# Performance work log

Hardware: AMD Instinct MI355X
Metric: run time of the kernel (lower is better)

## Reference

```python
import jax, jax.numpy as jnp
import numpy as np

EPS = 1e-6
STEPS = 6  # eval_steps == train_steps == 6


def _l2norm(v, axis, eps=1e-12):
    # F.normalize: v / max(||v||, eps)
    return v / jnp.maximum(jnp.linalg.norm(v, axis=axis, keepdims=True), eps)


def _conv1x1(x, w, b=None):
    # x: [B,C,H,W], w: [O,C]
    y = jnp.einsum('bchw,oc->bohw', x, w)
    if b is not None:
        y = y + b[None, :, None, None]
    return y


def _nmf_local_inference(x, bases):
    # x: [B,D,N], bases: [B,D,R]; torch.no_grad loop
    coef = jax.nn.softmax(jnp.einsum('bdn,bdr->bnr', x, bases), axis=-1)  # inv_t = 1

    def step(carry, _):
        bases, coef = carry
        # coef update
        xtb = jnp.einsum('bdn,bdr->bnr', x, bases)
        btb = jnp.einsum('bdr,bds->brs', bases, bases)
        coef = coef * xtb / (jnp.einsum('bnr,brs->bns', coef, btb) + EPS)
        # bases update
        xc = jnp.einsum('bdn,bnr->bdr', x, coef)
        ctc = jnp.einsum('bnr,bns->brs', coef, coef)
        bases = bases * xc / (jnp.einsum('bdr,brs->bds', bases, ctc) + EPS)
        return (bases, coef), None

    (bases, coef), _ = jax.lax.scan(step, (bases, coef), None, length=STEPS)
    return bases, coef


def _nmf_compute_coef(x, bases, coef):
    # differentiable final coef refinement
    xtb = jnp.einsum('bdn,bdr->bnr', x, bases)
    btb = jnp.einsum('bdr,bds->brs', bases, bases)
    return coef * xtb / (jnp.einsum('bnr,brs->bns', coef, btb) + EPS)


def _ham_nmf(h, bases0):
    # h: [B,C,H,W], S=1 -> D=C, N=H*W
    B, C, H, W = h.shape
    x = h.reshape(B, C, H * W)
    sg = jax.lax.stop_gradient
    bases, coef = _nmf_local_inference(sg(x), bases0)
    bases, coef = sg(bases), sg(coef)
    coef = _nmf_compute_coef(x, bases, coef)
    out = jnp.einsum('bdr,bnr->bdn', bases, coef)  # bases @ coef^T
    return out.reshape(B, C, H, W)


def reference(x, bases0, w_lower, b_lower, w_cheese, b_cheese, w_upper,
              coef_shortcut, coef_ham):
    shortcut = x
    # lower bread: 1x1 conv + ReLU (NMF variant)
    h = jax.nn.relu(_conv1x1(x, w_lower, b_lower))
    # hamburger (NMF2D, spatial=True, rand_init bases normalized over D)
    bases = _l2norm(bases0, axis=1)
    h = _ham_nmf(h, bases)
    # cheese: 1x1 conv + ReLU (norm_cfg=None -> conv has bias)
    h = jax.nn.relu(_conv1x1(h, w_cheese, b_cheese))
    # upper bread: 1x1 conv, no bias
    h = _conv1x1(h, w_upper)
    return jax.nn.relu(coef_ham * h + coef_shortcut * shortcut)


def setup_inputs() -> dict:
    key = jax.random.key(0)
    ks = jax.random.split(key, 8)
    B, in_c, Hh, Ww = 8, 512, 64, 64
    C, R = 512, 64
    std = (2.0 / C) ** 0.5  # kaiming-style init from _init_weight (1x1 convs)
    std_up = (2.0 / in_c) ** 0.5
    return {
        'x': jax.random.normal(ks[0], (B, in_c, Hh, Ww), jnp.float32),
        'bases0': jax.random.uniform(ks[1], (B, C, R), jnp.float32),
        'w_lower': jax.random.normal(ks[2], (C, in_c), jnp.float32) * std,
        'b_lower': jnp.zeros((C,), jnp.float32),
        'w_cheese': jax.random.normal(ks[3], (C, C), jnp.float32) * std,
        'b_cheese': jnp.zeros((C,), jnp.float32),
        'w_upper': jax.random.normal(ks[4], (in_c, C), jnp.float32) * std_up,
        'coef_shortcut': jnp.ones((1,), jnp.float32),
        'coef_ham': jnp.ones((1,), jnp.float32),
    }
```

## Files before the change

### kernel.cpp

```cpp
#include <hip/hip_runtime.h>

#define NMF_EPS 1e-6f

typedef unsigned short ushort_t;
typedef __attribute__((ext_vector_type(8))) short bf16x8;
typedef __attribute__((ext_vector_type(4))) float f32x4;

__device__ __forceinline__ ushort_t f2bf(float f) {
    unsigned int u = __float_as_uint(f);
    return (ushort_t)((u + 0x7FFFu + ((u >> 16) & 1u)) >> 16);
}
__device__ __forceinline__ float bf2f(ushort_t h) {
    return __uint_as_float(((unsigned int)h) << 16);
}

__device__ __forceinline__ void gl_lds16(const ushort_t* g, ushort_t* l) {
    __builtin_amdgcn_global_load_lds(
        (const __attribute__((address_space(1))) unsigned int*)g,
        (__attribute__((address_space(3))) unsigned int*)l,
        16, 0, 0);
}

template<int SPLIT, int EPI>
__global__ __launch_bounds__(256) void mfma_gemm(
    const ushort_t* __restrict__ Ah, const ushort_t* __restrict__ Al,
    const ushort_t* __restrict__ Bh, const ushort_t* __restrict__ Bl,
    float* __restrict__ C, ushort_t* __restrict__ Chi, ushort_t* __restrict__ Clo,
    int M, int N, int K,
    long sB, long sC,
    const float* __restrict__ bias,
    const float* __restrict__ res, long sRes,
    const float* __restrict__ hamp, const float* __restrict__ scp)
{
    constexpr int SB = SPLIT ? 32768 : 16384;
    __shared__ char smem[2 * SB];

    const int tid  = threadIdx.x;
    const int wave = tid >> 6, lane = tid & 63;
    const int quad = lane >> 4, lr = lane & 15;
    const int batch = blockIdx.z;
    const int m0 = blockIdx.y * 128, n0 = blockIdx.x * 128;

    const ushort_t* Bhb = Bh + (long)batch * sB;
    const ushort_t* Blb = SPLIT ? (Bl + (long)batch * sB) : nullptr;

    f32x4 acc[4][4];
    #pragma unroll
    for (int i = 0; i < 4; ++i)
        #pragma unroll
        for (int j = 0; j < 4; ++j)
            acc[i][j] = (f32x4){0.f, 0.f, 0.f, 0.f};

    const int q   = wave * 2;
    const int ra0 = (q + 0) * 16 + (lane >> 2);
    const int ra1 = (q + 1) * 16 + (lane >> 2);
    const int ko  = (lane & 3) * 8;
    const int wm = (wave & 1) * 64, wn = (wave >> 1) * 64;

    auto STAGE = [&](int buf, int k0) {
        char* base = smem + buf * SB;
        ushort_t* dAh = (ushort_t*)base;
        ushort_t* dBh = (ushort_t*)(base + 8192);
        gl_lds16(&Ah [(long)(m0 + ra0) * K + k0 + ko], &dAh[(q + 0) * 512]);
        gl_lds16(&Ah [(long)(m0 + ra1) * K + k0 + ko], &dAh[(q + 1) * 512]);
        gl_lds16(&Bhb[(long)(n0 + ra0) * K + k0 + ko], &dBh[(q + 0) * 512]);
        gl_lds16(&Bhb[(long)(n0 + ra1) * K + k0 + ko], &dBh[(q + 1) * 512]);
        if constexpr (SPLIT) {
            ushort_t* dAl = (ushort_t*)(base + 16384);
            ushort_t* dBl = (ushort_t*)(base + 24576);
            gl_lds16(&Al [(long)(m0 + ra0) * K + k0 + ko], &dAl[(q + 0) * 512]);
            gl_lds16(&Al [(long)(m0 + ra1) * K + k0 + ko], &dAl[(q + 1) * 512]);
            gl_lds16(&Blb[(long)(n0 + ra0) * K + k0 + ko], &dBl[(q + 0) * 512]);
            gl_lds16(&Blb[(long)(n0 + ra1) * K + k0 + ko], &dBl[(q + 1) * 512]);
        }
    };

    STAGE(0, 0);
    __syncthreads();
    int cur = 0;

    for (int k0 = 0; k0 < K; k0 += 32) {
        if (k0 + 32 < K) STAGE(cur ^ 1, k0 + 32);

        char* base = smem + cur * SB;
        ushort_t* sAh = (ushort_t*)base;
        ushort_t* sBh = (ushort_t*)(base + 8192);

        bf16x8 af[4], bfr[4], afl[4], bfl[4];
        #pragma unroll
        for (int i = 0; i < 4; ++i)
            af[i] = *(const bf16x8*)&sAh[(wm + i * 16 + lr) * 32 + quad * 8];
        #pragma unroll
        for (int j = 0; j < 4; ++j)
            bfr[j] = *(const bf16x8*)&sBh[(wn + j * 16 + lr) * 32 + quad * 8];
        if constexpr (SPLIT) {
            ushort_t* sAl = (ushort_t*)(base + 16384);
            ushort_t* sBl = (ushort_t*)(base + 24576);
            #pragma unroll
            for (int i = 0; i < 4; ++i)
                afl[i] = *(const bf16x8*)&sAl[(wm + i * 16 + lr) * 32 + quad * 8];
            #pragma unroll
            for (int j = 0; j < 4; ++j)
                bfl[j] = *(const bf16x8*)&sBl[(wn + j * 16 + lr) * 32 + quad * 8];
        }

        #pragma unroll
        for (int i = 0; i < 4; ++i)
            #pragma unroll
            for (int j = 0; j < 4; ++j) {
                acc[i][j] = __builtin_amdgcn_mfma_f32_16x16x32_bf16(af[i], bfr[j], acc[i][j], 0, 0, 0);
                if constexpr (SPLIT) {
                    acc[i][j] = __builtin_amdgcn_mfma_f32_16x16x32_bf16(af[i], bfl[j], acc[i][j], 0, 0, 0);
                    acc[i][j] = __builtin_amdgcn_mfma_f32_16x16x32_bf16(afl[i], bfr[j], acc[i][j], 0, 0, 0);
                }
            }
        __syncthreads();
        cur ^= 1;
    }

    if (EPI == 2) {
        ushort_t* Hh = Chi + (long)batch * sC;
        ushort_t* Hl = Clo + (long)batch * sC;
        unsigned int* slab = (unsigned int*)smem;
        #pragma unroll
        for (int p = 0; p < 2; ++p) {
            __syncthreads();
            if ((wave & 1) == p) {
                #pragma unroll
                for (int i = 0; i < 4; ++i) {
                    const int mb = m0 + p * 64 + i * 16 + quad * 4;
                    #pragma unroll
                    for (int j = 0; j < 4; ++j) {
                        const int nl = wn + j * 16 + lr;
                        #pragma unroll
                        for (int r = 0; r < 4; ++r) {
                            float v = fmaxf(acc[i][j][r] + bias[mb + r], 0.f);
                            ushort_t h = f2bf(v);
                            ushort_t l = f2bf(v - bf2f(h));
                            slab[nl * 64 + (i * 16 + quad * 4 + r)] =
                                (unsigned)h | ((unsigned)l << 16);
                        }
                    }
                }
            }
            __syncthreads();
            for (int idx = tid; idx < 8192; idx += 256) {
                const int nl = idx >> 6, ml = idx & 63;
                unsigned u = slab[idx];
                const long off = (long)(n0 + nl) * M + m0 + p * 64 + ml;
                Hh[off] = (ushort_t)(u & 0xffffu);
                Hl[off] = (ushort_t)(u >> 16);
            }
        }
    } else {
        const float hm = *hamp, sc = *scp;
        float* Cb = C + (long)batch * sC;
        #pragma unroll
        for (int i = 0; i < 4; ++i) {
            #pragma unroll
            for (int j = 0; j < 4; ++j) {
                const int mbase = m0 + wm + i * 16 + quad * 4;
                const int n     = n0 + wn + j * 16 + lr;
                #pragma unroll
                for (int r = 0; r < 4; ++r) {
                    float rv = res[(long)batch * sRes + (long)(mbase + r) * N + n];
                    Cb[(long)(mbase + r) * N + n] = fmaxf(fmaf(hm, acc[i][j][r], sc * rv), 0.f);
                }
            }
        }
    }
}

template<int MODE>
__global__ __launch_bounds__(256) void coef_step(
    const ushort_t* __restrict__ Xh, const ushort_t* __restrict__ Xl,
    const ushort_t* __restrict__ bth, const ushort_t* __restrict__ btl,
    const float* __restrict__ btb_part,
    float* __restrict__ coef,
    ushort_t* __restrict__ cth,
    float* __restrict__ ctc_part,
    int Bcnt)
{
    constexpr bool MU = (MODE >= 1);
    __shared__ char smem[32768 + 18432];
    ushort_t* stg = (ushort_t*)smem;
    ushort_t* gLh = (ushort_t*)(smem + 32768);
    ushort_t* gLl = gLh + 64 * 72;

    const int tid = threadIdx.x, wave = tid >> 6, lane = tid & 63;
    const int quad = lane >> 4, lr = lane & 15;
    const int b = blockIdx.y, n0 = blockIdx.x * 64;

    const ushort_t* Xhb  = Xh  + (long)b * 2097152 + (long)n0 * 512;
    const ushort_t* Xlb  = Xl  + (long)b * 2097152 + (long)n0 * 512;
    const ushort_t* bthb = bth + (long)b * 32768;
    const ushort_t* btlb = btl + (long)b * 32768;
    float* coefB = coef + (long)b * 262144 + (long)n0 * 64;

    if (MU) {
        for (int i = tid; i < 4096; i += 256) {
            const int r = i >> 6, s = i & 63;
            float v = 0.f;
            #pragma unroll
            for (int c = 0; c < 8; ++c)
                v += btb_part[((long)c * Bcnt + b) * 4096 + i];
            ushort_t h = f2bf(v);
            gLh[r * 72 + s] = h;
            gLl[r * 72 + s] = f2bf(v - bf2f(h));
        }
    }

    const int srow = wave * 16 + (lane >> 2);
    const int koff = (lane & 3) * 8;
    f32x4 accx[4];
    #pragma unroll
    for (int j = 0; j < 4; ++j) accx[j] = (f32x4){0.f, 0.f, 0.f, 0.f};

    if constexpr (MODE == 1) {
        auto STG = [&](int buf, int p) {
            const int kg0 = (2 * p) * 32 + koff;
            const int kg1 = (2 * p + 1) * 32 + koff;
            gl_lds16(&Xhb [(long)srow * 512 + kg0], &stg[buf * 8192 + 0 * 2048 + wave * 512]);
            gl_lds16(&Xhb [(long)srow * 512 + kg1], &stg[buf * 8192 + 1 * 2048 + wave * 512]);
            gl_lds16(&bthb[(long)srow * 512 + kg0], &stg[buf * 8192 + 2 * 2048 + wave * 512]);
            gl_lds16(&bthb[(long)srow * 512 + kg1], &stg[buf * 8192 + 3 * 2048 + wave * 512]);
        };
        STG(0, 0);
        __syncthreads();
        int cur = 0;
        for (int p = 0; p < 8; ++p) {
            if (p + 1 < 8) STG(cur ^ 1, p + 1);
            #pragma unroll
            for (int k2 = 0; k2 < 2; ++k2) {
                bf16x8 ah = *(const bf16x8*)&stg[cur * 8192 + k2 * 2048 + (wave * 16 + lr) * 32 + quad * 8];
                #pragma unroll
                for (int j = 0; j < 4; ++j) {
                    bf16x8 bh = *(const bf16x8*)&stg[cur * 8192 + (2 + k2) * 2048 + (j * 16 + lr) * 32 + quad * 8];
                    accx[j] = __builtin_amdgcn_mfma_f32_16x16x32_bf16(ah, bh, accx[j], 0, 0, 0);
                }
            }
            __syncthreads();
            cur ^= 1;
        }
    } else {
        auto STG = [&](int buf, int kc) {
            const int kg = kc * 32 + koff;
            gl_lds16(&Xhb [(long)srow * 512 + kg], &stg[buf * 8192 + 0 * 2048 + wave * 512]);
            gl_lds16(&Xlb [(long)srow * 512 + kg], &stg[buf * 8192 + 1 * 2048 + wave * 512]);
            gl_lds16(&bthb[(long)srow * 512 + kg], &stg[buf * 8192 + 2 * 2048 + wave * 512]);
            gl_lds16(&btlb[(long)srow * 512 + kg], &stg[buf * 8192 + 3 * 2048 + wave * 512]);
        };
        STG(0, 0);
        __syncthreads();
        int cur = 0;
        for (int kc = 0; kc < 16; ++kc) {
            if (kc + 1 < 16) STG(cur ^ 1, kc + 1);
            bf16x8 ah = *(const bf16x8*)&stg[cur * 8192 + 0 * 2048 + (wave * 16 + lr) * 32 + quad * 8];
            bf16x8 al = *(const bf16x8*)&stg[cur * 8192 + 1 * 2048 + (wave * 16 + lr) * 32 + quad * 8];
            #pragma unroll
            for (int j = 0; j < 4; ++j) {
                bf16x8 bh = *(const bf16x8*)&stg[cur * 8192 + 2 * 2048 + (j * 16 + lr) * 32 + quad * 8];
                bf16x8 bl = *(const bf16x8*)&stg[cur * 8192 + 3 * 2048 + (j * 16 + lr) * 32 + quad * 8];
                accx[j] = __builtin_amdgcn_mfma_f32_16x16x32_bf16(ah, bh, accx[j], 0, 0, 0);
                accx[j] = __builtin_amdgcn_mfma_f32_16x16x32_bf16(ah, bl, accx[j], 0, 0, 0);
                accx[j] = __builtin_amdgcn_mfma_f32_16x16x32_bf16(al, bh, accx[j], 0, 0, 0);
            }
            __syncthreads();
            cur ^= 1;
        }
    }

    float cnew[4][4];
    if (MU) {
        f32x4 accd[4];
        #pragma unroll
        for (int j = 0; j < 4; ++j) accd[j] = (f32x4){0.f, 0.f, 0.f, 0.f};
        #pragma unroll
        for (int kk = 0; kk < 2; ++kk) {
            const float* cp = &coefB[(wave * 16 + lr) * 64 + kk * 32 + quad * 8];
            float4 cA = *(const float4*)cp;
            float4 cB = *(const float4*)(cp + 4);
            float cv[8] = {cA.x, cA.y, cA.z, cA.w, cB.x, cB.y, cB.z, cB.w};
            bf16x8 ah, al;
            #pragma unroll
            for (int e = 0; e < 8; ++e) {
                ushort_t h = f2bf(cv[e]);
                ((short*)&ah)[e] = (short)h;
                ((short*)&al)[e] = (short)f2bf(cv[e] - bf2f(h));
            }
            #pragma unroll
            for (int j = 0; j < 4; ++j) {
                bf16x8 bh = *(const bf16x8*)&gLh[(j * 16 + lr) * 72 + kk * 32 + quad * 8];
                bf16x8 bl = *(const bf16x8*)&gLl[(j * 16 + lr) * 72 + kk * 32 + quad * 8];
                accd[j] = __builtin_amdgcn_mfma_f32_16x16x32_bf16(ah, bh, accd[j], 0, 0, 0);
                accd[j] = __builtin_amdgcn_mfma_f32_16x16x32_bf16(ah, bl, accd[j], 0, 0, 0);
                accd[j] = __builtin_amdgcn_mfma_f32_16x16x32_bf16(al, bh, accd[j], 0, 0, 0);
            }
        }
        #pragma unroll
        for (int j = 0; j < 4; ++j)
            #pragma unroll
            for (int r = 0; r < 4; ++r) {
                float cold = coefB[(wave * 16 + quad * 4 + r) * 64 + j * 16 + lr];
                cnew[j][r] = cold * accx[j][r] / (accd[j][r] + NMF_EPS);
            }
    } else {
        #pragma unroll
        for (int r = 0; r < 4; ++r) {
            float m = fmaxf(fmaxf(accx[0][r], accx[1][r]), fmaxf(accx[2][r], accx[3][r]));
            #pragma unroll
            for (int off = 1; off < 16; off <<= 1) m = fmaxf(m, __shfl_xor(m, off, 64));
            float e[4], s = 0.f;
            #pragma unroll
            for (int j = 0; j < 4; ++j) { e[j] = __expf(accx[j][r] - m); s += e[j]; }
            #pragma unroll
            for (int off = 1; off < 16; off <<= 1) s += __shfl_xor(s, off, 64);
            float inv = 1.f / s;
            #pragma unroll
            for (int j = 0; j < 4; ++j) cnew[j][r] = e[j] * inv;
        }
    }

    #pragma unroll
    for (int j = 0; j < 4; ++j)
        #pragma unroll
        for (int r = 0; r < 4; ++r)
            coefB[(wave * 16 + quad * 4 + r) * 64 + j * 16 + lr] = cnew[j][r];

    if (MODE != 1) return;

    __syncthreads();
    #pragma unroll
    for (int j = 0; j < 4; ++j)
        #pragma unroll
        for (int r = 0; r < 4; ++r) {
            const int nl = wave * 16 + quad * 4 + r;
            const int rr = j * 16 + lr;
            gLh[rr * 72 + nl] = f2bf(cnew[j][r]);
        }
    __syncthreads();
    for (int i = tid; i < 4096; i += 256) {
        const int r = i >> 6, nn = i & 63;
        cth[(long)b * 262144 + (long)r * 4096 + n0 + nn] = gLh[r * 72 + nn];
    }
    f32x4 accc[4];
    #pragma unroll
    for (int j = 0; j < 4; ++j) accc[j] = (f32x4){0.f, 0.f, 0.f, 0.f};
    #pragma unroll
    for (int kk = 0; kk < 64; kk += 32) {
        bf16x8 ah = *(const bf16x8*)&gLh[(wave * 16 + lr) * 72 + kk + quad * 8];
        #pragma unroll
        for (int j = 0; j < 4; ++j) {
            bf16x8 bh = *(const bf16x8*)&gLh[(j * 16 + lr) * 72 + kk + quad * 8];
            accc[j] = __builtin_amdgcn_mfma_f32_16x16x32_bf16(ah, bh, accc[j], 0, 0, 0);
        }
    }
    float* cp = ctc_part + ((long)blockIdx.x * Bcnt + b) * 4096;
    #pragma unroll
    for (int j = 0; j < 4; ++j)
        #pragma unroll
        for (int r = 0; r < 4; ++r)
            cp[(wave * 16 + quad * 4 + r) * 64 + j * 16 + lr] = accc[j][r];
}

__global__ __launch_bounds__(256) void xc_partial(
    const ushort_t* __restrict__ Ah,
    const ushort_t* __restrict__ Bh,
    float* __restrict__ part,
    const float* __restrict__ ctc_part,
    float* __restrict__ ctc,
    int Bcnt)
{
    __shared__ ushort_t stg[2 * 8192];
    const int tid = threadIdx.x;
    const int batch = blockIdx.z;

    if (blockIdx.y == 8) {
        const int i0 = blockIdx.x * 512;
        #pragma unroll
        for (int rep = 0; rep < 2; ++rep) {
            const int i = i0 + rep * 256 + tid;
            float v = 0.f;
            #pragma unroll 8
            for (int c = 0; c < 64; ++c)
                v += ctc_part[((long)c * Bcnt + batch) * 4096 + i];
            ctc[(long)batch * 4096 + i] = v;
        }
        return;
    }

    const int wave = tid >> 6, lane = tid & 63;
    const int quad = lane >> 4, lr = lane & 15;
    const int m0 = blockIdx.y * 64;
    const int k0 = blockIdx.x * 512;

    const ushort_t* Ab = Ah + (long)batch * 2097152;
    const ushort_t* Bb = Bh + (long)batch * 262144;

    const int srow = wave * 16 + (lane >> 2);
    const int koff = (lane & 3) * 8;

    f32x4 acc[4];
    #pragma unroll
    for (int j = 0; j < 4; ++j) acc[j] = (f32x4){0.f, 0.f, 0.f, 0.f};

    auto STG = [&](int buf, int p) {
        const int kg0 = k0 + (2 * p) * 32 + koff;
        const int kg1 = k0 + (2 * p + 1) * 32 + koff;
        gl_lds16(&Ab[(long)(m0 + srow) * 4096 + kg0], &stg[buf * 8192 + 0 * 2048 + wave * 512]);
        gl_lds16(&Ab[(long)(m0 + srow) * 4096 + kg1], &stg[buf * 8192 + 1 * 2048 + wave * 512]);
        gl_lds16(&Bb[(long)srow * 4096 + kg0], &stg[buf * 8192 + 2 * 2048 + wave * 512]);
        gl_lds16(&Bb[(long)srow * 4096 + kg1], &stg[buf * 8192 + 3 * 2048 + wave * 512]);
    };

    STG(0, 0);
    __syncthreads();
    int cur = 0;

    for (int p = 0; p < 8; ++p) {
        if (p + 1 < 8) STG(cur ^ 1, p + 1);
        #pragma unroll
        for (int k2 = 0; k2 < 2; ++k2) {
            bf16x8 ah = *(const bf16x8*)&stg[cur * 8192 + k2 * 2048 + (wave * 16 + lr) * 32 + quad * 8];
            #pragma unroll
            for (int j = 0; j < 4; ++j) {
                bf16x8 bh = *(const bf16x8*)&stg[cur * 8192 + (2 + k2) * 2048 + (j * 16 + lr) * 32 + quad * 8];
                acc[j] = __builtin_amdgcn_mfma_f32_16x16x32_bf16(ah, bh, acc[j], 0, 0, 0);
            }
        }
        __syncthreads();
        cur ^= 1;
    }

    float* Cb = part + ((long)blockIdx.x * Bcnt + batch) * 32768;
    #pragma unroll
    for (int j = 0; j < 4; ++j) {
        const int col = j * 16 + lr;
        #pragma unroll
        for (int r = 0; r < 4; ++r)
            Cb[(long)(m0 + wave * 16 + quad * 4 + r) * 64 + col] = acc[j][r];
    }
}

template<int MODE>
__global__ __launch_bounds__(256) void bases_step(
    const float* __restrict__ xc_part,
    const float* __restrict__ ctc,
    float* __restrict__ bases,
    ushort_t* __restrict__ bth, ushort_t* __restrict__ btl,
    float* __restrict__ btb_part,
    int Bcnt)
{
    __shared__ char smem[16640 * 2 + 18432];
    float* bnL  = (float*)smem;
    float* ctcL = (float*)(smem + 16640);
    ushort_t* btLh = (ushort_t*)(smem + 33280);
    ushort_t* btLl = btLh + 64 * 72;
    float* basesL = (float*)(smem + 33280);

    const int b = blockIdx.y, c0 = blockIdx.x * 64;
    const int tid = threadIdx.x;
    float* basesB = bases + (long)b * 32768 + (long)c0 * 64;

    if (MODE == 1) {
        for (int i = tid; i < 4096; i += 256) {
            const int c = i >> 6, r = i & 63;
            basesL[c * 65 + r] = basesB[i];
            ctcL[c * 65 + r]   = ctc[(long)b * 4096 + i];
            float v = 0.f;
            #pragma unroll
            for (int s0 = 0; s0 < 8; ++s0)
                v += xc_part[((long)s0 * Bcnt + b) * 32768 + (long)(c0 + c) * 64 + r];
            bnL[c * 65 + r] = v;
        }
        __syncthreads();
        for (int i = tid; i < 4096; i += 256) {
            const int c = i >> 6, r = i & 63;
            float denom = 0.f;
            #pragma unroll 8
            for (int s = 0; s < 64; ++s)
                denom = fmaf(basesL[c * 65 + s], ctcL[s * 65 + r], denom);
            float bnew = basesL[c * 65 + r] * bnL[c * 65 + r] / (denom + NMF_EPS);
            bnL[c * 65 + r] = bnew;
            basesB[i] = bnew;
        }
        __syncthreads();
    } else {
        for (int i = tid; i < 4096; i += 256)
            bnL[(i >> 6) * 65 + (i & 63)] = basesB[i];
        __syncthreads();
    }

    for (int i = tid; i < 4096; i += 256) {
        const int r = i >> 6, cc = i & 63;
        float v = bnL[cc * 65 + r];
        ushort_t h = f2bf(v);
        ushort_t l = f2bf(v - bf2f(h));
        btLh[r * 72 + cc] = h;
        btLl[r * 72 + cc] = l;
        bth[(long)b * 32768 + (long)r * 512 + c0 + cc] = h;
        btl[(long)b * 32768 + (long)r * 512 + c0 + cc] = l;
    }
    __syncthreads();

    const int wave = tid >> 6, lane = tid & 63;
    const int quad = lane >> 4, lr = lane & 15;
    f32x4 acg[4];
    #pragma unroll
    for (int j = 0; j < 4; ++j) acg[j] = (f32x4){0.f, 0.f, 0.f, 0.f};
    #pragma unroll
    for (int kk = 0; kk < 64; kk += 32) {
        bf16x8 ah = *(const bf16x8*)&btLh[(wave * 16 + lr) * 72 + kk + quad * 8];
        bf16x8 al = *(const bf16x8*)&btLl[(wave * 16 + lr) * 72 + kk + quad * 8];
        #pragma unroll
        for (int j = 0; j < 4; ++j) {
            bf16x8 bh = *(const bf16x8*)&btLh[(j * 16 + lr) * 72 + kk + quad * 8];
            bf16x8 bl = *(const bf16x8*)&btLl[(j * 16 + lr) * 72 + kk + quad * 8];
            acg[j] = __builtin_amdgcn_mfma_f32_16x16x32_bf16(ah, bh, acg[j], 0, 0, 0);
            acg[j] = __builtin_amdgcn_mfma_f32_16x16x32_bf16(ah, bl, acg[j], 0, 0, 0);
            acg[j] = __builtin_amdgcn_mfma_f32_16x16x32_bf16(al, bh, acg[j], 0, 0, 0);
        }
    }
    float* gp = btb_part + ((long)blockIdx.x * Bcnt + b) * 4096;
    #pragma unroll
    for (int j = 0; j < 4; ++j)
        #pragma unroll
        for (int r = 0; r < 4; ++r)
            gp[(wave * 16 + quad * 4 + r) * 64 + j * 16 + lr] = acg[j][r];
}

constexpr int BM = 64, BN = 64, BK = 16;

template<int ALAY, int BLAY, int EPI>
__global__ __launch_bounds__(256) void gemm_kernel(
    const float* __restrict__ A, const float* __restrict__ B, float* __restrict__ C,
    int Kchunk, int kchunks,
    int lda, int ldb, int ldc,
    long sA, long sB, long sC,
    const float* __restrict__ bias)
{
    __shared__ float As[BK][BM + 4];
    __shared__ float Bs[BK][BN + 4];

    const int batch = blockIdx.z;
    const float* Ab = A + (long)batch * sA;
    const float* Bb = B + (long)batch * sB;

    const int m0  = blockIdx.y * BM;
    const int n0  = blockIdx.x * BN;
    const int tid = threadIdx.x;
    const int ty  = tid >> 4, tx = tid & 15;

    float acc[4][4] = {};

    for (int kt = 0; kt < Kchunk; kt += BK) {
        if (ALAY == 0) {
            const int m = tid >> 2, k4 = (tid & 3) << 2;
            float4 v = *(const float4*)&Ab[(long)(m0 + m) * lda + (kt + k4)];
            As[k4 + 0][m] = v.x; As[k4 + 1][m] = v.y;
            As[k4 + 2][m] = v.z; As[k4 + 3][m] = v.w;
        } else {
            const int k = tid >> 4, m4 = (tid & 15) << 2;
            float4 v = *(const float4*)&Ab[(long)(kt + k) * lda + (m0 + m4)];
            *(float4*)&As[k][m4] = v;
        }
        if (BLAY == 0) {
            const int k = tid >> 4, n4 = (tid & 15) << 2;
            float4 v = *(const float4*)&Bb[(long)(kt + k) * ldb + (n0 + n4)];
            *(float4*)&Bs[k][n4] = v;
        } else {
            const int n = tid >> 2, k4 = (tid & 3) << 2;
            float4 v = *(const float4*)&Bb[(long)(n0 + n) * ldb + (kt + k4)];
            Bs[k4 + 0][n] = v.x; Bs[k4 + 1][n] = v.y;
            Bs[k4 + 2][n] = v.z; Bs[k4 + 3][n] = v.w;
        }
        __syncthreads();
        #pragma unroll
        for (int k = 0; k < BK; ++k) {
            float4 a4 = *(const float4*)&As[k][ty << 2];
            float4 b4 = *(const float4*)&Bs[k][tx << 2];
            float av[4] = {a4.x, a4.y, a4.z, a4.w};
            float bv[4] = {b4.x, b4.y, b4.z, b4.w};
            #pragma unroll
            for (int i = 0; i < 4; ++i)
                #pragma unroll
                for (int j = 0; j < 4; ++j)
                    acc[i][j] = fmaf(av[i], bv[j], acc[i][j]);
        }
        __syncthreads();
    }

    const int mb = m0 + (ty << 2), nb = n0 + (tx << 2);
    if (EPI == 4) {
        ushort_t* Cu = (ushort_t*)C + (long)batch * sC;
        #pragma unroll
        for (int j = 0; j < 4; ++j) {
            ushort_t pk[4];
            #pragma unroll
            for (int i = 0; i < 4; ++i)
                pk[i] = f2bf(fmaxf(acc[i][j] + bias[mb + i], 0.f));
            *(ushort4*)&Cu[(long)(nb + j) * ldc + mb] =
                make_ushort4(pk[0], pk[1], pk[2], pk[3]);
        }
    } else {
        float* Cb = C + (long)batch * sC;
        #pragma unroll
        for (int i = 0; i < 4; ++i) {
            float4 o = make_float4(acc[i][0], acc[i][1], acc[i][2], acc[i][3]);
            *(float4*)&Cb[(long)(mb + i) * ldc + nb] = o;
        }
    }
}

__global__ __launch_bounds__(256) void cast_x_t(const float* __restrict__ x,
                                                ushort_t* __restrict__ hi,
                                                ushort_t* __restrict__ lo)
{
    __shared__ float t[64][65];
    const int b = blockIdx.z, c0 = blockIdx.y * 64, n0 = blockIdx.x * 64;
    const int tid = threadIdx.x, tx = tid & 63, ty = tid >> 6;
    const float* xb = x + (long)b * 512 * 4096;
    #pragma unroll 4
    for (int s = ty; s < 64; s += 4)
        t[s][tx] = xb[(long)(c0 + s) * 4096 + n0 + tx];
    __syncthreads();
    #pragma unroll 4
    for (int s = ty; s < 64; s += 4) {
        float v = t[tx][s];
        long idx = (long)b * 2097152 + (long)(n0 + s) * 512 + c0 + tx;
        ushort_t h = f2bf(v);
        hi[idx] = h;
        lo[idx] = f2bf(v - bf2f(h));
    }
}

__global__ __launch_bounds__(256) void nd2dn(const ushort_t* __restrict__ hi,
                                             ushort_t* __restrict__ dhi)
{
    __shared__ ushort_t t[64][66];
    const int b = blockIdx.z, n0 = blockIdx.x * 64, c0 = blockIdx.y * 64;
    const int tx = threadIdx.x & 63, ty = threadIdx.x >> 6;
    const long base = (long)b * 2097152;
    #pragma unroll 4
    for (int s = ty; s < 64; s += 4) {
        long idx = base + (long)(n0 + s) * 512 + c0 + tx;
        t[s][tx] = hi[idx];
    }
    __syncthreads();
    #pragma unroll 4
    for (int s = ty; s < 64; s += 4) {
        long idx = base + (long)(c0 + s) * 4096 + n0 + tx;
        dhi[idx] = t[tx][s];
    }
}

__global__ __launch_bounds__(256) void prep256(
    const float* __restrict__ w_lower, ushort_t* __restrict__ wl_hi, ushort_t* __restrict__ wl_lo,
    const float* __restrict__ w_upper, ushort_t* __restrict__ w_up,
    const float* __restrict__ b0, float* __restrict__ bases)
{
    const int bx = blockIdx.x, tid = threadIdx.x;
    if (bx < 1024) {
        int i = bx * 256 + tid;
        float v = w_lower[i];
        ushort_t h = f2bf(v);
        wl_hi[i] = h;
        wl_lo[i] = f2bf(v - bf2f(h));
        return;
    }
    if (bx < 2048) {
        int i = (bx - 1024) * 256 + tid;
        w_up[i] = f2bf(w_upper[i]);
        return;
    }
    __shared__ float part[4][64];
    const int b = bx - 2048;
    const int r = tid & 63, slice = tid >> 6;
    const float* src = b0 + (long)b * 512 * 64;
    float* dst = bases + (long)b * 512 * 64;
    float s = 0.f;
    #pragma unroll 8
    for (int d = slice; d < 512; d += 4) {
        float v = src[d * 64 + r];
        s = fmaf(v, v, s);
    }
    part[slice][r] = s;
    __syncthreads();
    if (slice == 0) {
        float t = part[0][r] + part[1][r] + part[2][r] + part[3][r];
        part[0][r] = 1.0f / fmaxf(sqrtf(t), 1e-12f);
    }
    __syncthreads();
    const float inv = part[0][r];
    #pragma unroll 8
    for (int d = slice; d < 512; d += 4)
        dst[d * 64 + r] = src[d * 64 + r] * inv;
}

extern "C" void kernel_launch(void* const* d_in, const int* in_sizes, int n_in,
                              void* d_out, int out_size, void* d_ws, size_t ws_size,
                              hipStream_t stream)
{
    const float* x_in     = (const float*)d_in[0];
    const float* bases0   = (const float*)d_in[1];
    const float* w_lower  = (const float*)d_in[2];
    const float* b_lower  = (const float*)d_in[3];
    const float* w_cheese = (const float*)d_in[4];
    const float* b_cheese = (const float*)d_in[5];
    const float* w_upper  = (const float*)d_in[6];
    const float* csc      = (const float*)d_in[7];
    const float* cham     = (const float*)d_in[8];
    float* out = (float*)d_out;

    const int B = 8, C = 512, N = 4096, R = 64;
    const long sCN = (long)C * N;
    const long sNC = (long)N * C;
    const long sNR = (long)N * R, sCR = (long)C * R;

    char* w = (char*)d_ws;
    ushort_t* X_nd_hi  = (ushort_t*)w;  w += 33554432;
    ushort_t* xt_hi    = (ushort_t*)w;  w += 33554432;
    ushort_t* xt_lo    = (ushort_t*)w;  w += 33554432;
    float*    coef     = (float*)w;     w += 8388608;
    ushort_t* ct_hi    = (ushort_t*)w;  w += 4194304;
    float*    ctc_part = (float*)w;     w += 8388608;
    float*    xc_part  = (float*)w;     w += 8388608;
    float*    btb_part = (float*)w;     w += 1048576;
    float*    bases    = (float*)w;     w += 1048576;
    float*    WcB      = (float*)w;     w += 1048576;
    float*    ctc      = (float*)w;     w += 131072;
    ushort_t* bt_hi    = (ushort_t*)w;  w += 524288;
    ushort_t* bt_lo    = (ushort_t*)w;  w += 524288;
    ushort_t* wl_hi    = (ushort_t*)w;  w += 524288;
    ushort_t* wl_lo    = (ushort_t*)w;  w += 524288;
    ushort_t* w_up     = (ushort_t*)w;  w += 524288;

    ushort_t* X_nd_lo;
    {
        const size_t used = (size_t)(w - (char*)d_ws);
        if (ws_size >= used + 33554432UL) {
            X_nd_lo = (ushort_t*)w;  w += 33554432;
        } else {
            X_nd_lo = (ushort_t*)d_out;
        }
    }

    ushort_t* X_dn_hi  = xt_hi;
    ushort_t* cheese_t = X_nd_hi;

    const dim3 blk(256);

    prep256<<<dim3(2056), blk, 0, stream>>>(w_lower, wl_hi, wl_lo, w_upper, w_up,
                                            bases0, bases);
    bases_step<0><<<dim3(C / 64, B), blk, 0, stream>>>(
        nullptr, nullptr, bases, bt_hi, bt_lo, btb_part, B);
    cast_x_t<<<dim3(N / 64, C / 64, B), blk, 0, stream>>>(x_in, xt_hi, xt_lo);

    mfma_gemm<1, 2><<<dim3(N / 128, C / 128, B), blk, 0, stream>>>(
        wl_hi, wl_lo, xt_hi, xt_lo, nullptr, X_nd_hi, X_nd_lo,
        C, N, C, sNC, sNC, b_lower, nullptr, 0L, nullptr, nullptr);
    nd2dn<<<dim3(N / 64, C / 64, B), blk, 0, stream>>>(X_nd_hi, X_dn_hi);

    coef_step<0><<<dim3(N / 64, B), blk, 0, stream>>>(
        X_nd_hi, X_nd_lo, bt_hi, bt_lo, btb_part, coef, ct_hi, ctc_part, B);

    for (int step = 0; step < 6; ++step) {
        coef_step<1><<<dim3(N / 64, B), blk, 0, stream>>>(
            X_nd_hi, X_nd_lo, bt_hi, bt_lo, btb_part, coef, ct_hi, ctc_part, B);
        xc_partial<<<dim3(8, 9, B), blk, 0, stream>>>(
            X_dn_hi, ct_hi, xc_part, ctc_part, ctc, B);
        bases_step<1><<<dim3(C / 64, B), blk, 0, stream>>>(
            xc_part, ctc, bases, bt_hi, bt_lo, btb_part, B);
    }

    coef_step<2><<<dim3(N / 64, B), blk, 0, stream>>>(
        X_nd_hi, X_nd_lo, bt_hi, bt_lo, btb_part, coef, ct_hi, ctc_part, B);

    gemm_kernel<0, 0, 0><<<dim3(1, C / BM, B), blk, 0, stream>>>(
        w_cheese, bases, WcB, C, 1, C, R, R, 0L, sCR, sCR, nullptr);
    gemm_kernel<0, 1, 4><<<dim3(N / BN, C / BM, B), blk, 0, stream>>>(
        WcB, coef, (float*)cheese_t, R, 1, R, R, C, sCR, sNR, sNC, b_cheese);

    mfma_gemm<0, 3><<<dim3(N / 128, C / 128, B), blk, 0, stream>>>(
        w_up, nullptr, cheese_t, nullptr, out, nullptr, nullptr,
        C, N, C, sNC, sCN, nullptr, x_in, sCN, cham, csc);
}
```

Before: 653.2 us.

## Move cheese GEMM to split-bf16 MFMA and drop low part of lower weights

The cheese 1x1 conv (WcB @ coef) moves off the scalar fp32 gemm_kernel and onto the MFMA GEMM. The final coef_step now writes coef as bf16 hi/lo pairs, and the WcB product is emitted as a hi/lo bf16 split, so the 3-term split MFMA keeps near-fp32 accuracy. The lower conv also drops the low half of the weight split (new SPLIT=2 mode: two MFMAs instead of three, less LDS traffic), trading a little precision on w_lower for fewer matrix ops. Buffers are reused by aliasing ct_hi and ctc_part for the coef hi/lo outputs.

```diff
diff --git a/kernel.cpp b/kernel.cpp
--- a/kernel.cpp
+++ b/kernel.cpp
@@ -27,12 +27,12 @@
     const ushort_t* __restrict__ Bh, const ushort_t* __restrict__ Bl,
     float* __restrict__ C, ushort_t* __restrict__ Chi, ushort_t* __restrict__ Clo,
     int M, int N, int K,
-    long sB, long sC,
+    long sA, long sB, long sC,
     const float* __restrict__ bias,
     const float* __restrict__ res, long sRes,
     const float* __restrict__ hamp, const float* __restrict__ scp)
 {
-    constexpr int SB = SPLIT ? 32768 : 16384;
+    constexpr int SB = (SPLIT == 1) ? 32768 : (SPLIT == 2) ? 24576 : 16384;
     __shared__ char smem[2 * SB];
 
     const int tid  = threadIdx.x;
@@ -41,8 +41,10 @@
     const int batch = blockIdx.z;
     const int m0 = blockIdx.y * 128, n0 = blockIdx.x * 128;
 
+    const ushort_t* Ahb = Ah + (long)batch * sA;
+    const ushort_t* Alb = (SPLIT == 1) ? (Al + (long)batch * sA) : nullptr;
     const ushort_t* Bhb = Bh + (long)batch * sB;
-    const ushort_t* Blb = SPLIT ? (Bl + (long)batch * sB) : nullptr;
+    const ushort_t* Blb = (SPLIT >= 1) ? (Bl + (long)batch * sB) : nullptr;
 
     f32x4 acc[4][4];
     #pragma unroll
@@ -61,15 +63,19 @@
         char* base = smem + buf * SB;
         ushort_t* dAh = (ushort_t*)base;
         ushort_t* dBh = (ushort_t*)(base + 8192);
-        gl_lds16(&Ah [(long)(m0 + ra0) * K + k0 + ko], &dAh[(q + 0) * 512]);
-        gl_lds16(&Ah [(long)(m0 + ra1) * K + k0 + ko], &dAh[(q + 1) * 512]);
+        gl_lds16(&Ahb[(long)(m0 + ra0) * K + k0 + ko], &dAh[(q + 0) * 512]);
+        gl_lds16(&Ahb[(long)(m0 + ra1) * K + k0 + ko], &dAh[(q + 1) * 512]);
         gl_lds16(&Bhb[(long)(n0 + ra0) * K + k0 + ko], &dBh[(q + 0) * 512]);
         gl_lds16(&Bhb[(long)(n0 + ra1) * K + k0 + ko], &dBh[(q + 1) * 512]);
-        if constexpr (SPLIT) {
+        if constexpr (SPLIT == 1) {
             ushort_t* dAl = (ushort_t*)(base + 16384);
             ushort_t* dBl = (ushort_t*)(base + 24576);
-            gl_lds16(&Al [(long)(m0 + ra0) * K + k0 + ko], &dAl[(q + 0) * 512]);
-            gl_lds16(&Al [(long)(m0 + ra1) * K + k0 + ko], &dAl[(q + 1) * 512]);
+            gl_lds16(&Alb[(long)(m0 + ra0) * K + k0 + ko], &dAl[(q + 0) * 512]);
+            gl_lds16(&Alb[(long)(m0 + ra1) * K + k0 + ko], &dAl[(q + 1) * 512]);
+            gl_lds16(&Blb[(long)(n0 + ra0) * K + k0 + ko], &dBl[(q + 0) * 512]);
+            gl_lds16(&Blb[(long)(n0 + ra1) * K + k0 + ko], &dBl[(q + 1) * 512]);
+        } else if constexpr (SPLIT == 2) {
+            ushort_t* dBl = (ushort_t*)(base + 16384);
             gl_lds16(&Blb[(long)(n0 + ra0) * K + k0 + ko], &dBl[(q + 0) * 512]);
             gl_lds16(&Blb[(long)(n0 + ra1) * K + k0 + ko], &dBl[(q + 1) * 512]);
         }
@@ -93,7 +99,7 @@
         #pragma unroll
         for (int j = 0; j < 4; ++j)
             bfr[j] = *(const bf16x8*)&sBh[(wn + j * 16 + lr) * 32 + quad * 8];
-        if constexpr (SPLIT) {
+        if constexpr (SPLIT == 1) {
             ushort_t* sAl = (ushort_t*)(base + 16384);
             ushort_t* sBl = (ushort_t*)(base + 24576);
             #pragma unroll
@@ -102,6 +108,11 @@
             #pragma unroll
             for (int j = 0; j < 4; ++j)
                 bfl[j] = *(const bf16x8*)&sBl[(wn + j * 16 + lr) * 32 + quad * 8];
+        } else if constexpr (SPLIT == 2) {
+            ushort_t* sBl = (ushort_t*)(base + 16384);
+            #pragma unroll
+            for (int j = 0; j < 4; ++j)
+                bfl[j] = *(const bf16x8*)&sBl[(wn + j * 16 + lr) * 32 + quad * 8];
         }
 
         #pragma unroll
@@ -109,18 +120,20 @@
             #pragma unroll
             for (int j = 0; j < 4; ++j) {
                 acc[i][j] = __builtin_amdgcn_mfma_f32_16x16x32_bf16(af[i], bfr[j], acc[i][j], 0, 0, 0);
-                if constexpr (SPLIT) {
+                if constexpr (SPLIT == 1) {
                     acc[i][j] = __builtin_amdgcn_mfma_f32_16x16x32_bf16(af[i], bfl[j], acc[i][j], 0, 0, 0);
                     acc[i][j] = __builtin_amdgcn_mfma_f32_16x16x32_bf16(afl[i], bfr[j], acc[i][j], 0, 0, 0);
+                } else if constexpr (SPLIT == 2) {
+                    acc[i][j] = __builtin_amdgcn_mfma_f32_16x16x32_bf16(af[i], bfl[j], acc[i][j], 0, 0, 0);
                 }
             }
         __syncthreads();
         cur ^= 1;
     }
 
-    if (EPI == 2) {
+    if (EPI == 2 || EPI == 5) {
         ushort_t* Hh = Chi + (long)batch * sC;
-        ushort_t* Hl = Clo + (long)batch * sC;
+        ushort_t* Hl = (EPI == 2) ? (Clo + (long)batch * sC) : nullptr;
         unsigned int* slab = (unsigned int*)smem;
         #pragma unroll
         for (int p = 0; p < 2; ++p) {
@@ -136,9 +149,12 @@
                         for (int r = 0; r < 4; ++r) {
                             float v = fmaxf(acc[i][j][r] + bias[mb + r], 0.f);
                             ushort_t h = f2bf(v);
-                            ushort_t l = f2bf(v - bf2f(h));
-                            slab[nl * 64 + (i * 16 + quad * 4 + r)] =
-                                (unsigned)h | ((unsigned)l << 16);
+                            unsigned uu = (unsigned)h;
+                            if (EPI == 2) {
+                                ushort_t l = f2bf(v - bf2f(h));
+                                uu |= ((unsigned)l << 16);
+                            }
+                            slab[nl * 64 + (i * 16 + quad * 4 + r)] = uu;
                         }
                     }
                 }
@@ -149,7 +165,7 @@
                 unsigned u = slab[idx];
                 const long off = (long)(n0 + nl) * M + m0 + p * 64 + ml;
                 Hh[off] = (ushort_t)(u & 0xffffu);
-                Hl[off] = (ushort_t)(u >> 16);
+                if (EPI == 2) Hl[off] = (ushort_t)(u >> 16);
             }
         }
     } else {
@@ -179,6 +195,7 @@
     float* __restrict__ coef,
     ushort_t* __restrict__ cth,
     float* __restrict__ ctc_part,
+    ushort_t* __restrict__ cfh, ushort_t* __restrict__ cfl,
     int Bcnt)
 {
     constexpr bool MU = (MODE >= 1);
@@ -321,6 +338,22 @@
         }
     }
 
+    if constexpr (MODE == 2) {
+        ushort_t* cfhB = cfh + (long)b * 262144 + (long)n0 * 64;
+        ushort_t* cflB = cfl + (long)b * 262144 + (long)n0 * 64;
+        #pragma unroll
+        for (int j = 0; j < 4; ++j)
+            #pragma unroll
+            for (int r = 0; r < 4; ++r) {
+                const long idx = (long)(wave * 16 + quad * 4 + r) * 64 + j * 16 + lr;
+                float v = cnew[j][r];
+                ushort_t h = f2bf(v);
+                cfhB[idx] = h;
+                cflB[idx] = f2bf(v - bf2f(h));
+            }
+        return;
+    }
+
     #pragma unroll
     for (int j = 0; j < 4; ++j)
         #pragma unroll
@@ -591,17 +624,17 @@
     }
 
     const int mb = m0 + (ty << 2), nb = n0 + (tx << 2);
-    if (EPI == 4) {
+    if (EPI == 5) {
         ushort_t* Cu = (ushort_t*)C + (long)batch * sC;
         #pragma unroll
-        for (int j = 0; j < 4; ++j) {
-            ushort_t pk[4];
-            #pragma unroll
-            for (int i = 0; i < 4; ++i)
-                pk[i] = f2bf(fmaxf(acc[i][j] + bias[mb + i], 0.f));
-            *(ushort4*)&Cu[(long)(nb + j) * ldc + mb] =
-                make_ushort4(pk[0], pk[1], pk[2], pk[3]);
-        }
+        for (int i = 0; i < 4; ++i)
+            #pragma unroll
+            for (int j = 0; j < 4; ++j) {
+                float v = acc[i][j];
+                ushort_t h = f2bf(v);
+                Cu[(long)(mb + i) * ldc + (nb + j)] = h;
+                Cu[32768 + (long)(mb + i) * ldc + (nb + j)] = f2bf(v - bf2f(h));
+            }
     } else {
         float* Cb = C + (long)batch * sC;
         #pragma unroll
@@ -655,17 +688,14 @@
 }
 
 __global__ __launch_bounds__(256) void prep256(
-    const float* __restrict__ w_lower, ushort_t* __restrict__ wl_hi, ushort_t* __restrict__ wl_lo,
+    const float* __restrict__ w_lower, ushort_t* __restrict__ wl_hi,
     const float* __restrict__ w_upper, ushort_t* __restrict__ w_up,
     const float* __restrict__ b0, float* __restrict__ bases)
 {
     const int bx = blockIdx.x, tid = threadIdx.x;
     if (bx < 1024) {
         int i = bx * 256 + tid;
-        float v = w_lower[i];
-        ushort_t h = f2bf(v);
-        wl_hi[i] = h;
-        wl_lo[i] = f2bf(v - bf2f(h));
+        wl_hi[i] = f2bf(w_lower[i]);
         return;
     }
     if (bx < 2048) {
@@ -715,7 +745,7 @@
     const int B = 8, C = 512, N = 4096, R = 64;
     const long sCN = (long)C * N;
     const long sNC = (long)N * C;
-    const long sNR = (long)N * R, sCR = (long)C * R;
+    const long sCR = (long)C * R;
 
     char* w = (char*)d_ws;
     ushort_t* X_nd_hi  = (ushort_t*)w;  w += 33554432;
@@ -727,7 +757,7 @@
     float*    xc_part  = (float*)w;     w += 8388608;
     float*    btb_part = (float*)w;     w += 1048576;
     float*    bases    = (float*)w;     w += 1048576;
-    float*    WcB      = (float*)w;     w += 1048576;
+    ushort_t* WcBu     = (ushort_t*)w;  w += 1048576;
     float*    ctc      = (float*)w;     w += 131072;
     ushort_t* bt_hi    = (ushort_t*)w;  w += 524288;
     ushort_t* bt_lo    = (ushort_t*)w;  w += 524288;
@@ -747,26 +777,30 @@
 
     ushort_t* X_dn_hi  = xt_hi;
     ushort_t* cheese_t = X_nd_hi;
+    ushort_t* coef_hi  = ct_hi;
+    ushort_t* coef_lo  = (ushort_t*)ctc_part;
 
     const dim3 blk(256);
 
-    prep256<<<dim3(2056), blk, 0, stream>>>(w_lower, wl_hi, wl_lo, w_upper, w_up,
+    prep256<<<dim3(2056), blk, 0, stream>>>(w_lower, wl_hi, w_upper, w_up,
                                             bases0, bases);
     bases_step<0><<<dim3(C / 64, B), blk, 0, stream>>>(
         nullptr, nullptr, bases, bt_hi, bt_lo, btb_part, B);
     cast_x_t<<<dim3(N / 64, C / 64, B), blk, 0, stream>>>(x_in, xt_hi, xt_lo);
 
-    mfma_gemm<1, 2><<<dim3(N / 128, C / 128, B), blk, 0, stream>>>(
-        wl_hi, wl_lo, xt_hi, xt_lo, nullptr, X_nd_hi, X_nd_lo,
-        C, N, C, sNC, sNC, b_lower, nullptr, 0L, nullptr, nullptr);
+    mfma_gemm<2, 2><<<dim3(N / 128, C / 128, B), blk, 0, stream>>>(
+        wl_hi, nullptr, xt_hi, xt_lo, nullptr, X_nd_hi, X_nd_lo,
+        C, N, C, 0L, sNC, sNC, b_lower, nullptr, 0L, nullptr, nullptr);
     nd2dn<<<dim3(N / 64, C / 64, B), blk, 0, stream>>>(X_nd_hi, X_dn_hi);
 
     coef_step<0><<<dim3(N / 64, B), blk, 0, stream>>>(
-        X_nd_hi, X_nd_lo, bt_hi, bt_lo, btb_part, coef, ct_hi, ctc_part, B);
+        X_nd_hi, X_nd_lo, bt_hi, bt_lo, btb_part, coef, ct_hi, ctc_part,
+        nullptr, nullptr, B);
 
     for (int step = 0; step < 6; ++step) {
         coef_step<1><<<dim3(N / 64, B), blk, 0, stream>>>(
-            X_nd_hi, X_nd_lo, bt_hi, bt_lo, btb_part, coef, ct_hi, ctc_part, B);
+            X_nd_hi, X_nd_lo, bt_hi, bt_lo, btb_part, coef, ct_hi, ctc_part,
+            nullptr, nullptr, B);
         xc_partial<<<dim3(8, 9, B), blk, 0, stream>>>(
             X_dn_hi, ct_hi, xc_part, ctc_part, ctc, B);
         bases_step<1><<<dim3(C / 64, B), blk, 0, stream>>>(
@@ -774,14 +808,16 @@
     }
 
     coef_step<2><<<dim3(N / 64, B), blk, 0, stream>>>(
-        X_nd_hi, X_nd_lo, bt_hi, bt_lo, btb_part, coef, ct_hi, ctc_part, B);
-
-    gemm_kernel<0, 0, 0><<<dim3(1, C / BM, B), blk, 0, stream>>>(
-        w_cheese, bases, WcB, C, 1, C, R, R, 0L, sCR, sCR, nullptr);
-    gemm_kernel<0, 1, 4><<<dim3(N / BN, C / BM, B), blk, 0, stream>>>(
-        WcB, coef, (float*)cheese_t, R, 1, R, R, C, sCR, sNR, sNC, b_cheese);
+        X_nd_hi, X_nd_lo, bt_hi, bt_lo, btb_part, coef, nullptr, nullptr,
+        coef_hi, coef_lo, B);
+
+    gemm_kernel<0, 0, 5><<<dim3(1, C / BM, B), blk, 0, stream>>>(
+        w_cheese, bases, (float*)WcBu, C, 1, C, R, R, 0L, sCR, 65536L, nullptr);
+    mfma_gemm<1, 5><<<dim3(N / 128, C / 128, B), blk, 0, stream>>>(
+        WcBu, WcBu + 32768, coef_hi, coef_lo, nullptr, cheese_t, nullptr,
+        C, N, R, 65536L, (long)N * R, sNC, b_cheese, nullptr, 0L, nullptr, nullptr);
 
     mfma_gemm<0, 3><<<dim3(N / 128, C / 128, B), blk, 0, stream>>>(
         w_up, nullptr, cheese_t, nullptr, out, nullptr, nullptr,
-        C, N, C, sNC, sCN, nullptr, x_in, sCN, cham, csc);
-}
+        C, N, C, 0L, sNC, sCN, nullptr, x_in, sCN, cham, csc);
+}
```

Result: slower. 695.8 us (+6.5%).
